# Performance work log

Measured on AMD Instinct MI355X. Metric: run time of the kernel, lower is better.

## Reference

```python
import jax, jax.numpy as jnp
import numpy as np

N_FFT = 2048
HOP = 512
WIN = 2048
PAD = N_FFT // 2  # center padding, n_fft // 2


def setup_inputs() -> dict:
    key = jax.random.key(0)
    x = jax.random.normal(key, (16, 262144), dtype=jnp.float32)
    # periodic Hann window, identical to torch.hann_window(2048)
    window = (0.5 - 0.5 * jnp.cos(2.0 * jnp.pi * jnp.arange(WIN) / WIN)).astype(jnp.float32)
    return {"x": x, "window": window}


def reference(x, window):
    # x: [B, T]; center reflect-pad by n_fft//2 on both sides (matches F.pad mode='reflect')
    xp = jnp.pad(x, ((0, 0), (PAD, PAD)), mode="reflect")
    n_frames = (xp.shape[-1] - N_FFT) // HOP + 1  # static
    # strided framing (replaces the identity-conv im2col in the original)
    idx = jnp.arange(n_frames)[:, None] * HOP + jnp.arange(N_FFT)[None, :]  # [F, n_fft]
    frames = xp[:, idx] * window  # [B, F, n_fft], windowed frames
    # windowed DFT; rfft of windowed frame == F.linear(frames, fft_k) in the original
    spec = jnp.fft.rfft(frames, axis=-1)  # [B, F, n_fft//2+1] complex
    real = jnp.real(spec).transpose(0, 2, 1)  # [B, dim, F]
    imag = jnp.imag(spec).transpose(0, 2, 1)  # [B, dim, F]
    return (real, imag)
```

## Files before the change

### kernel.cpp

```cpp
#include <hip/hip_runtime.h>


#define N_FFT   2048
#define LOG2N   11
#define HOP     512
#define PADL    1024
#define NBINS   1025
#define NFRAMES 513
#define NBATCH  16
#define TLEN    262144

#define HALF_OUT ((size_t)NBATCH * NBINS * NFRAMES)

__device__ __forceinline__ int pidx(int a) { return a + (a >> 5); }

__device__ __forceinline__ int refl(int j) {
    if (j < 0)          j = -j;
    else if (j >= TLEN) j = 2 * TLEN - 2 - j;
    return j;
}

__device__ __forceinline__ float2 cmul(float2 a, float2 w) {
    return make_float2(fmaf(a.x, w.x, -a.y * w.y), fmaf(a.x, w.y, a.y * w.x));
}
__device__ __forceinline__ float2 cadd(float2 a, float2 b) {
    return make_float2(a.x + b.x, a.y + b.y);
}
__device__ __forceinline__ float2 csub(float2 a, float2 b) {
    return make_float2(a.x - b.x, a.y - b.y);
}
__device__ __forceinline__ float2 csqr(float2 w) {
    return make_float2(fmaf(w.x, w.x, -w.y * w.y), 2.0f * w.x * w.y);
}

template <int H, int L2H>
__device__ __forceinline__ void octet_pass(float2* __restrict__ zc, int q) {
    const int p    = q & (H - 1);
    const int base = ((q >> L2H) << (L2H + 3)) + p;
    int ia[8];
#pragma unroll
    for (int m = 0; m < 8; ++m) ia[m] = pidx(base + m * H);
    float2 v0 = zc[ia[0]], v1 = zc[ia[1]], v2 = zc[ia[2]], v3 = zc[ia[3]];
    float2 v4 = zc[ia[4]], v5 = zc[ia[5]], v6 = zc[ia[6]], v7 = zc[ia[7]];

    float2 w1, w2, w3;
    if (H == 1) {
        w3 = make_float2(1.0f, 0.0f); w2 = w3; w1 = w3;
    } else {
        float s, c;
        __sincosf((float)p * (-3.14159265358979323846f / (4.0f * (float)H)), &s, &c);
        w3 = make_float2(c, s);
        w2 = csqr(w3);
        w1 = csqr(w2);
    }

    float2 t;
    t = cmul(v1, w1); v1 = csub(v0, t); v0 = cadd(v0, t);
    t = cmul(v3, w1); v3 = csub(v2, t); v2 = cadd(v2, t);
    t = cmul(v5, w1); v5 = csub(v4, t); v4 = cadd(v4, t);
    t = cmul(v7, w1); v7 = csub(v6, t); v6 = cadd(v6, t);
    const float2 w2m = make_float2(w2.y, -w2.x);
    t = cmul(v2, w2);  v2 = csub(v0, t); v0 = cadd(v0, t);
    t = cmul(v3, w2m); v3 = csub(v1, t); v1 = cadd(v1, t);
    t = cmul(v6, w2);  v6 = csub(v4, t); v4 = cadd(v4, t);
    t = cmul(v7, w2m); v7 = csub(v5, t); v5 = cadd(v5, t);
    const float R = 0.70710678118654752f;
    const float2 w3o  = make_float2((w3.x + w3.y) * R, (w3.y - w3.x) * R);
    const float2 w3m  = make_float2(w3.y, -w3.x);
    const float2 w3mo = make_float2(w3o.y, -w3o.x);
    t = cmul(v4, w3);   v4 = csub(v0, t); v0 = cadd(v0, t);
    t = cmul(v5, w3o);  v5 = csub(v1, t); v1 = cadd(v1, t);
    t = cmul(v6, w3m);  v6 = csub(v2, t); v2 = cadd(v2, t);
    t = cmul(v7, w3mo); v7 = csub(v3, t); v3 = cadd(v3, t);

    zc[ia[0]] = v0; zc[ia[1]] = v1; zc[ia[2]] = v2; zc[ia[3]] = v3;
    zc[ia[4]] = v4; zc[ia[5]] = v5; zc[ia[6]] = v6; zc[ia[7]] = v7;
}

__global__ __launch_bounds__(1024) void stft_one(
    const float* __restrict__ x,
    const float* __restrict__ window,
    float* __restrict__ out)
{
    __shared__ float2 z[9][2112];

    const int d     = blockIdx.x + 32 * blockIdx.y;
    const int pair  = (d >> 4) * 8 + (d & 7);
    const int gg    = 2 * pair + ((d >> 3) & 1);
    const int b     = gg >> 5;
    const int g     = gg & 31;
    const int tid   = threadIdx.x;
    const int f0    = g * 16;
    const int nsub  = (g == 31) ? 9 : 8;

    const float* xb = x + (size_t)b * TLEN;
    for (int idx = tid; idx < nsub * 2048; idx += 1024) {
        const int c  = idx >> 11;
        const int n  = idx & 2047;
        const int fa = f0 + 2 * c;
        const float w  = window[n];
        const float va = xb[refl(fa * HOP - PADL + n)] * w;
        const float vb = xb[refl((fa + 1) * HOP - PADL + n)] * w;
        const int r = (int)(__brev((unsigned)n) >> (32 - LOG2N));
        z[c][pidx(r)] = make_float2(va, vb);
    }
    __syncthreads();

    for (int idx = tid; idx < nsub * 256; idx += 1024)
        octet_pass<1, 0>(z[idx >> 8], idx & 255);
    __syncthreads();
    for (int idx = tid; idx < nsub * 256; idx += 1024)
        octet_pass<8, 3>(z[idx >> 8], idx & 255);
    __syncthreads();
    for (int idx = tid; idx < nsub * 256; idx += 1024)
        octet_pass<64, 6>(z[idx >> 8], idx & 255);
    __syncthreads();

    for (int idx = tid; idx < nsub * 512; idx += 1024) {
        const int c = idx >> 9;
        const int p = idx & 511;
        float s, cc;
        __sincosf((float)p * (-3.14159265358979323846f / 1024.0f), &s, &cc);
        const float2 w2  = make_float2(cc, s);
        const float2 w1  = csqr(w2);
        const float2 w2m = make_float2(w2.y, -w2.x);
        const int i0 = pidx(p), i1 = pidx(p + 512), i2 = pidx(p + 1024), i3 = pidx(p + 1536);
        float2 v0 = z[c][i0], v1 = z[c][i1], v2 = z[c][i2], v3 = z[c][i3];
        float2 t;
        t = cmul(v1, w1); v1 = csub(v0, t); v0 = cadd(v0, t);
        t = cmul(v3, w1); v3 = csub(v2, t); v2 = cadd(v2, t);
        t = cmul(v2, w2);  v2 = csub(v0, t); v0 = cadd(v0, t);
        t = cmul(v3, w2m); v3 = csub(v1, t); v1 = cadd(v1, t);
        z[c][i0] = v0; z[c][i1] = v1; z[c][i2] = v2; z[c][i3] = v3;
    }
    __syncthreads();

    float* __restrict__ outr = out;
    float* __restrict__ outi = out + HALF_OUT;
    for (int k = tid; k < NBINS; k += 1024) {
        const int km = (N_FFT - k) & (N_FFT - 1);
        const size_t orow = ((size_t)b * NBINS + (size_t)k) * NFRAMES + (size_t)f0;
#pragma unroll
        for (int c = 0; c < 8; ++c) {
            const float2 zk = z[c][pidx(k)];
            const float2 zr = z[c][pidx(km)];
            outr[orow + 2 * c]     = 0.5f * (zk.x + zr.x);
            outr[orow + 2 * c + 1] = 0.5f * (zk.y + zr.y);
            outi[orow + 2 * c]     = 0.5f * (zk.y - zr.y);
            outi[orow + 2 * c + 1] = 0.5f * (zr.x - zk.x);
        }
        if (nsub == 9) {
            const float2 zk = z[8][pidx(k)];
            const float2 zr = z[8][pidx(km)];
            outr[orow + 16] = 0.5f * (zk.x + zr.x);
            outi[orow + 16] = 0.5f * (zk.y - zr.y);
        }
    }
}

extern "C" void kernel_launch(void* const* d_in, const int* in_sizes, int n_in,
                              void* d_out, int out_size, void* d_ws, size_t ws_size,
                              hipStream_t stream) {
    const float* x      = (const float*)d_in[0];
    const float* window = (const float*)d_in[1];
    float* out          = (float*)d_out;

    dim3 grid(32, NBATCH);
    stft_one<<<grid, 1024, 0, stream>>>(x, window, out);
}
```

Baseline: 127.3 us.

## Replace shared-memory FFT with register-resident four-step FFT per wavefront

Rewrites the STFT kernel so that each 64-lane wavefront computes one packed pair of frames entirely in registers. The FFT becomes a four-step scheme: a 32-point in-register FFT with constant twiddles, a twiddle multiply, and a 64-point cross-lane FFT built from shuffles. This drops shared memory and all block barriers. It also skips reflection indexing for interior frames, stores output as paired 2-float vectors, and remaps blocks across XCDs with a small tail grid. In exchange it needs heavy register use (32 complex values per lane) and many cross-lane shuffles, and the non-contiguous per-bin stores may coalesce poorly.

```diff
diff --git a/kernel.cpp b/kernel.cpp
--- a/kernel.cpp
+++ b/kernel.cpp
@@ -2,7 +2,6 @@
 
 
 #define N_FFT   2048
-#define LOG2N   11
 #define HOP     512
 #define PADL    1024
 #define NBINS   1025
@@ -12,7 +11,8 @@
 
 #define HALF_OUT ((size_t)NBATCH * NBINS * NFRAMES)
 
-__device__ __forceinline__ int pidx(int a) { return a + (a >> 5); }
+typedef float f2_t __attribute__((ext_vector_type(2)));
+typedef f2_t uf2 __attribute__((aligned(4)));
 
 __device__ __forceinline__ int refl(int j) {
     if (j < 0)          j = -j;
@@ -29,131 +29,145 @@
 __device__ __forceinline__ float2 csub(float2 a, float2 b) {
     return make_float2(a.x - b.x, a.y - b.y);
 }
-__device__ __forceinline__ float2 csqr(float2 w) {
-    return make_float2(fmaf(w.x, w.x, -w.y * w.y), 2.0f * w.x * w.y);
+
+__device__ __forceinline__ constexpr int BR5(int v) {
+    return ((v & 1) << 4) | ((v & 2) << 2) | (v & 4) | ((v & 8) >> 2) | ((v & 16) >> 4);
 }
 
-template <int H, int L2H>
-__device__ __forceinline__ void octet_pass(float2* __restrict__ zc, int q) {
-    const int p    = q & (H - 1);
-    const int base = ((q >> L2H) << (L2H + 3)) + p;
-    int ia[8];
-#pragma unroll
-    for (int m = 0; m < 8; ++m) ia[m] = pidx(base + m * H);
-    float2 v0 = zc[ia[0]], v1 = zc[ia[1]], v2 = zc[ia[2]], v3 = zc[ia[3]];
-    float2 v4 = zc[ia[4]], v5 = zc[ia[5]], v6 = zc[ia[6]], v7 = zc[ia[7]];
-
-    float2 w1, w2, w3;
-    if (H == 1) {
-        w3 = make_float2(1.0f, 0.0f); w2 = w3; w1 = w3;
-    } else {
-        float s, c;
-        __sincosf((float)p * (-3.14159265358979323846f / (4.0f * (float)H)), &s, &c);
-        w3 = make_float2(c, s);
-        w2 = csqr(w3);
-        w1 = csqr(w2);
-    }
-
-    float2 t;
-    t = cmul(v1, w1); v1 = csub(v0, t); v0 = cadd(v0, t);
-    t = cmul(v3, w1); v3 = csub(v2, t); v2 = cadd(v2, t);
-    t = cmul(v5, w1); v5 = csub(v4, t); v4 = cadd(v4, t);
-    t = cmul(v7, w1); v7 = csub(v6, t); v6 = cadd(v6, t);
-    const float2 w2m = make_float2(w2.y, -w2.x);
-    t = cmul(v2, w2);  v2 = csub(v0, t); v0 = cadd(v0, t);
-    t = cmul(v3, w2m); v3 = csub(v1, t); v1 = cadd(v1, t);
-    t = cmul(v6, w2);  v6 = csub(v4, t); v4 = cadd(v4, t);
-    t = cmul(v7, w2m); v7 = csub(v5, t); v5 = cadd(v5, t);
-    const float R = 0.70710678118654752f;
-    const float2 w3o  = make_float2((w3.x + w3.y) * R, (w3.y - w3.x) * R);
-    const float2 w3m  = make_float2(w3.y, -w3.x);
-    const float2 w3mo = make_float2(w3o.y, -w3o.x);
-    t = cmul(v4, w3);   v4 = csub(v0, t); v0 = cadd(v0, t);
-    t = cmul(v5, w3o);  v5 = csub(v1, t); v1 = cadd(v1, t);
-    t = cmul(v6, w3m);  v6 = csub(v2, t); v2 = cadd(v2, t);
-    t = cmul(v7, w3mo); v7 = csub(v3, t); v3 = cadd(v3, t);
-
-    zc[ia[0]] = v0; zc[ia[1]] = v1; zc[ia[2]] = v2; zc[ia[3]] = v3;
-    zc[ia[4]] = v4; zc[ia[5]] = v5; zc[ia[6]] = v6; zc[ia[7]] = v7;
-}
-
-__global__ __launch_bounds__(1024) void stft_one(
+__global__ __launch_bounds__(256) void stft_one(
     const float* __restrict__ x,
     const float* __restrict__ window,
     float* __restrict__ out)
 {
-    __shared__ float2 z[9][2112];
+    const int d   = blockIdx.x;
+    const int tid = threadIdx.x;
+    const int wv  = tid >> 6;
+    const int l   = tid & 63;
 
-    const int d     = blockIdx.x + 32 * blockIdx.y;
-    const int pair  = (d >> 4) * 8 + (d & 7);
-    const int gg    = 2 * pair + ((d >> 3) & 1);
-    const int b     = gg >> 5;
-    const int g     = gg & 31;
-    const int tid   = threadIdx.x;
-    const int f0    = g * 16;
-    const int nsub  = (g == 31) ? 9 : 8;
+    int b, pr; bool tail;
+    if (d < 4) {
+        b = d * 4 + wv; pr = 0; tail = true;
+    } else {
+        tail = false;
+        const int m    = d - 4;
+        const int xcd  = m & 7;
+        const int slot = m >> 3;
+        const int Q    = (slot >> 2) * 8 + xcd;
+        const int L    = Q * 4 + (slot & 3);
+        b  = L >> 6;
+        pr = (L & 63) * 4 + wv;
+    }
+    const int fa = tail ? 512 : 2 * pr;
+    const int a0 = fa * HOP - PADL;
+    const float* xb = x + (size_t)b * TLEN;
 
-    const float* xb = x + (size_t)b * TLEN;
-    for (int idx = tid; idx < nsub * 2048; idx += 1024) {
-        const int c  = idx >> 11;
-        const int n  = idx & 2047;
-        const int fa = f0 + 2 * c;
-        const float w  = window[n];
-        const float va = xb[refl(fa * HOP - PADL + n)] * w;
-        const float vb = xb[refl((fa + 1) * HOP - PADL + n)] * w;
-        const int r = (int)(__brev((unsigned)n) >> (32 - LOG2N));
-        z[c][pidx(r)] = make_float2(va, vb);
+    float2 u[32];
+    if (!tail && pr >= 1 && pr <= 254) {
+#pragma unroll
+        for (int r = 0; r < 32; ++r) {
+            const int n = l + 64 * r;
+            const float w = window[n];
+            u[r] = make_float2(xb[a0 + n] * w, xb[a0 + 512 + n] * w);
+        }
+    } else {
+#pragma unroll
+        for (int r = 0; r < 32; ++r) {
+            const int n = l + 64 * r;
+            const float w = window[n];
+            u[r] = make_float2(xb[refl(a0 + n)] * w, xb[refl(a0 + 512 + n)] * w);
+        }
     }
-    __syncthreads();
 
-    for (int idx = tid; idx < nsub * 256; idx += 1024)
-        octet_pass<1, 0>(z[idx >> 8], idx & 255);
-    __syncthreads();
-    for (int idx = tid; idx < nsub * 256; idx += 1024)
-        octet_pass<8, 3>(z[idx >> 8], idx & 255);
-    __syncthreads();
-    for (int idx = tid; idx < nsub * 256; idx += 1024)
-        octet_pass<64, 6>(z[idx >> 8], idx & 255);
-    __syncthreads();
+    {
+        constexpr float WC[16] = {
+            1.0f, 0.9807852804f, 0.9238795325f, 0.8314696123f,
+            0.7071067812f, 0.5555702330f, 0.3826834324f, 0.1950903220f,
+            0.0f, -0.1950903220f, -0.3826834324f, -0.5555702330f,
+            -0.7071067812f, -0.8314696123f, -0.9238795325f, -0.9807852804f };
+        constexpr float WS[16] = {
+            -0.0f, -0.1950903220f, -0.3826834324f, -0.5555702330f,
+            -0.7071067812f, -0.8314696123f, -0.9238795325f, -0.9807852804f,
+            -1.0f, -0.9807852804f, -0.9238795325f, -0.8314696123f,
+            -0.7071067812f, -0.5555702330f, -0.3826834324f, -0.1950903220f };
+#pragma unroll
+        for (int h = 16; h >= 1; h >>= 1) {
+#pragma unroll
+            for (int base = 0; base < 32; base += 2 * h) {
+#pragma unroll
+                for (int j = 0; j < h; ++j) {
+                    const int i = base + j;
+                    const float2 A = u[i], B = u[i + h];
+                    const int t = j * (16 / h);
+                    u[i]     = cadd(A, B);
+                    u[i + h] = cmul(csub(A, B), make_float2(WC[t], WS[t]));
+                }
+            }
+        }
+    }
 
-    for (int idx = tid; idx < nsub * 512; idx += 1024) {
-        const int c = idx >> 9;
-        const int p = idx & 511;
-        float s, cc;
-        __sincosf((float)p * (-3.14159265358979323846f / 1024.0f), &s, &cc);
-        const float2 w2  = make_float2(cc, s);
-        const float2 w1  = csqr(w2);
-        const float2 w2m = make_float2(w2.y, -w2.x);
-        const int i0 = pidx(p), i1 = pidx(p + 512), i2 = pidx(p + 1024), i3 = pidx(p + 1536);
-        float2 v0 = z[c][i0], v1 = z[c][i1], v2 = z[c][i2], v3 = z[c][i3];
-        float2 t;
-        t = cmul(v1, w1); v1 = csub(v0, t); v0 = cadd(v0, t);
-        t = cmul(v3, w1); v3 = csub(v2, t); v2 = cadd(v2, t);
-        t = cmul(v2, w2);  v2 = csub(v0, t); v0 = cadd(v0, t);
-        t = cmul(v3, w2m); v3 = csub(v1, t); v1 = cadd(v1, t);
-        z[c][i0] = v0; z[c][i1] = v1; z[c][i2] = v2; z[c][i3] = v3;
+    {
+        float s1, c1;
+        __sincosf(-3.14159265358979323846f / 1024.0f * (float)l, &s1, &c1);
+        const float2 t1 = make_float2(c1, s1);
+        float2 w = t1;
+#pragma unroll
+        for (int k2 = 1; k2 < 32; ++k2) {
+            u[BR5(k2)] = cmul(u[BR5(k2)], w);
+            w = cmul(w, t1);
+        }
     }
-    __syncthreads();
 
+#pragma unroll
+    for (int h = 32; h >= 1; h >>= 1) {
+        const int j = l & (h - 1);
+        float s3, c3;
+        __sincosf(-3.14159265358979323846f * (float)j / (float)h, &s3, &c3);
+        const bool hi = (l & h) != 0;
+        const float2 weff = hi ? make_float2(c3, s3) : make_float2(1.0f, 0.0f);
+#pragma unroll
+        for (int i = 0; i < 32; ++i) {
+            const float2 p = make_float2(__shfl_xor(u[i].x, h),
+                                         __shfl_xor(u[i].y, h));
+            const float2 t = hi ? csub(p, u[i]) : cadd(u[i], p);
+            u[i] = cmul(t, weff);
+        }
+    }
+
+    const int k1 = (int)(__brev((unsigned)l) >> 26);
+    const int kk = (64 - k1) & 63;
+    const int lp = (int)(__brev((unsigned)kk) >> 26);
+    const float2 xr0 = make_float2(__shfl(u[0].x, lp), __shfl(u[0].y, lp));
+    const bool ev = ((l & 1) == 0);
     float* __restrict__ outr = out;
     float* __restrict__ outi = out + HALF_OUT;
-    for (int k = tid; k < NBINS; k += 1024) {
-        const int km = (N_FFT - k) & (N_FFT - 1);
-        const size_t orow = ((size_t)b * NBINS + (size_t)k) * NFRAMES + (size_t)f0;
+
 #pragma unroll
-        for (int c = 0; c < 8; ++c) {
-            const float2 zk = z[c][pidx(k)];
-            const float2 zr = z[c][pidx(km)];
-            outr[orow + 2 * c]     = 0.5f * (zk.x + zr.x);
-            outr[orow + 2 * c + 1] = 0.5f * (zk.y + zr.y);
-            outi[orow + 2 * c]     = 0.5f * (zk.y - zr.y);
-            outi[orow + 2 * c + 1] = 0.5f * (zr.x - zk.x);
+    for (int p = 0; p < 32; ++p) {
+        const int k2 = BR5(p);
+        float2 xr;
+        if (p == 0) {
+            xr = xr0;
+        } else {
+            const int pp = BR5(32 - k2);
+            xr = make_float2(__shfl_xor(u[pp].x, 63), __shfl_xor(u[pp].y, 63));
         }
-        if (nsub == 9) {
-            const float2 zk = z[8][pidx(k)];
-            const float2 zr = z[8][pidx(km)];
-            outr[orow + 16] = 0.5f * (zk.x + zr.x);
-            outi[orow + 16] = 0.5f * (zk.y - zr.y);
+        const float2 xk = u[p];
+        const bool doSt = ev || (l == 1 && p == 0);
+        if (doSt) {
+            const int k = k2 + 32 * k1;
+            const size_t o = ((size_t)b * NBINS + (size_t)k) * NFRAMES + (size_t)fa;
+            if (!tail) {
+                uf2 re, im;
+                re.x = 0.5f * (xk.x + xr.x);
+                re.y = 0.5f * (xk.y + xr.y);
+                im.x = 0.5f * (xk.y - xr.y);
+                im.y = 0.5f * (xr.x - xk.x);
+                *reinterpret_cast<uf2*>(&outr[o]) = re;
+                *reinterpret_cast<uf2*>(&outi[o]) = im;
+            } else {
+                outr[o] = 0.5f * (xk.x + xr.x);
+                outi[o] = 0.5f * (xk.y - xr.y);
+            }
         }
     }
 }
@@ -165,6 +179,6 @@
     const float* window = (const float*)d_in[1];
     float* out          = (float*)d_out;
 
-    dim3 grid(32, NBATCH);
-    stft_one<<<grid, 1024, 0, stream>>>(x, window, out);
+    dim3 grid(1028);
+    stft_one<<<grid, 256, 0, stream>>>(x, window, out);
 }
```

After: 134.3 us. 5.5% more time.
